# Performance work log

Measured on AMD Instinct MI355X. Metric: run time of the kernel, lower is better.

The kernel has to match this reference:

```python
import jax, jax.numpy as jnp
import numpy as np

N_USERS = 50000
DEG = 32
N_EDGES = N_USERS * DEG  # 1,600,000
N_SERVERS = 512


def segment_softmax(x, seg, num_segments):
    # PyG-style scatter softmax over segments defined by seg.
    m = jax.ops.segment_max(x, seg, num_segments=num_segments)
    e = jnp.exp(x - m[seg])
    s = jax.ops.segment_sum(e, seg, num_segments=num_segments) + 1e-16
    return e / s[seg]


def setup_inputs() -> dict:
    key = jax.random.key(0)
    k1, k2, k3, k4, k5, k6, k7 = jax.random.split(key, 7)
    # learned parameters (torch.rand init), shape [E, 1]
    task_allocation = jax.random.uniform(k1, (N_EDGES, 1), dtype=jnp.float32)
    power_allocation = jax.random.uniform(k2, (N_EDGES, 1), dtype=jnp.float32)
    comp_allocation = jax.random.uniform(k3, (N_EDGES, 1), dtype=jnp.float32)
    compute_resource = jax.random.uniform(k4, (N_SERVERS,), dtype=jnp.float32) + 0.5
    path_losses = jax.random.uniform(k5, (N_EDGES,), dtype=jnp.float32) + 0.1
    task_size = jax.random.uniform(k6, (N_USERS,), dtype=jnp.float32) + 0.1
    # user index sorted (each user has DEG edges); server index random
    user_index = jnp.repeat(jnp.arange(N_USERS, dtype=jnp.int64), DEG)
    server_index = jax.random.randint(k7, (N_EDGES,), 0, N_SERVERS, dtype=jnp.int64)
    edge_index = jnp.stack([user_index, server_index], axis=0)
    return {
        "compute_resource": compute_resource,
        "path_losses": path_losses,
        "task_size": task_size,
        "edge_index": edge_index,
        "task_allocation": task_allocation,
        "power_allocation": power_allocation,
        "comp_allocation": comp_allocation,
    }


def reference(compute_resource, path_losses, task_size, edge_index,
              task_allocation, power_allocation, comp_allocation):
    epsilon = 1e-9
    extre = 1e-20
    n_users = task_size.shape[0]
    n_servers = compute_resource.shape[0]
    user_index = edge_index[0]
    server_index = edge_index[1]

    task_sche = segment_softmax(task_allocation[:, 0], user_index, n_users)
    power_sche = segment_softmax(power_allocation[:, 0], user_index, n_users)
    comp_sche = segment_softmax(comp_allocation[:, 0], user_index, n_users)

    tasks = task_size[user_index] * task_sche            # [E]
    comp = compute_resource[server_index] * comp_sche     # [E]
    pw = power_sche * path_losses                         # [E]

    # per-server total received power, broadcast back to edges
    pws = jax.ops.segment_sum(pw, server_index, num_segments=n_servers)[server_index]
    interference = pws - pw
    rate = jnp.log2(1.0 + pw / (interference + epsilon))

    time_loss = tasks / (rate + extre) + tasks / (comp + extre)  # [E]
    per_user = jax.ops.segment_sum(time_loss, user_index, num_segments=n_users)
    return per_user.mean()
```

## Files before the change

kernel.cpp:

```cpp
#include <hip/hip_runtime.h>
#include <math.h>

#define NSRV 512
#define NB1  256

__device__ __forceinline__ float quad_sum(float v) {
    int x = __float_as_int(v);
    int y = __builtin_amdgcn_update_dpp(0, x, 0xB1, 0xF, 0xF, true);
    v += __int_as_float(y);
    x = __float_as_int(v);
    y = __builtin_amdgcn_update_dpp(0, x, 0x4E, 0xF, 0xF, true);
    v += __int_as_float(y);
    return v;
}

__device__ __forceinline__ float fast_rcp(float x) {
    return __builtin_amdgcn_rcpf(x);
}

__global__ __launch_bounds__(256) void mmse_pws(
    const float* __restrict__ power_alloc,
    const float* __restrict__ path_losses,
    const int*   __restrict__ server_index,
    float*       __restrict__ pws,
    int n_items) {
    __shared__ float bins[NSRV];
    const int tid = threadIdx.x;
    for (int i = tid; i < NSRV; i += 256) bins[i] = 0.0f;
    __syncthreads();

    const float4* pa4 = (const float4*)power_alloc;
    const float4* pl4 = (const float4*)path_losses;
    const int4*   si4 = (const int4*)server_index;

    const int stride = NB1 * 256;
    for (int t = blockIdx.x * 256 + tid; t < n_items; t += stride) {
        float4 a = pa4[2 * t], b = pa4[2 * t + 1];
        float e0 = __expf(a.x), e1 = __expf(a.y), e2 = __expf(a.z), e3 = __expf(a.w);
        float e4 = __expf(b.x), e5 = __expf(b.y), e6 = __expf(b.z), e7 = __expf(b.w);
        float s   = ((e0 + e1) + (e2 + e3)) + ((e4 + e5) + (e6 + e7));
        float inv = fast_rcp(quad_sum(s) + 1e-16f);

        float4 l0 = pl4[2 * t], l1 = pl4[2 * t + 1];
        int4   s0 = si4[2 * t], s1 = si4[2 * t + 1];

        atomicAdd(&bins[s0.x], e0 * inv * l0.x);
        atomicAdd(&bins[s0.y], e1 * inv * l0.y);
        atomicAdd(&bins[s0.z], e2 * inv * l0.z);
        atomicAdd(&bins[s0.w], e3 * inv * l0.w);
        atomicAdd(&bins[s1.x], e4 * inv * l1.x);
        atomicAdd(&bins[s1.y], e5 * inv * l1.y);
        atomicAdd(&bins[s1.z], e6 * inv * l1.z);
        atomicAdd(&bins[s1.w], e7 * inv * l1.w);
    }
    __syncthreads();

    for (int i = tid; i < NSRV; i += 256) atomicAdd(&pws[i], bins[i]);
}

__global__ __launch_bounds__(256) void mmse_loss(
    const float* __restrict__ task_alloc,
    const float* __restrict__ power_alloc,
    const float* __restrict__ comp_alloc,
    const float* __restrict__ path_losses,
    const int*   __restrict__ server_index,
    const float* __restrict__ task_size,
    const float* __restrict__ compute_resource,
    const float* __restrict__ pws,
    float*       __restrict__ out,
    int n_items, float inv_users) {
    __shared__ float s_pws[NSRV], s_cr[NSRV];
    __shared__ float s_blocksum;
    const int tid = threadIdx.x;

    for (int i = tid; i < NSRV; i += 256) {
        s_pws[i] = pws[i];
        s_cr[i]  = compute_resource[i];
    }
    if (tid == 0) s_blocksum = 0.0f;
    __syncthreads();

    const int t = blockIdx.x * 256 + tid;
    float tl = 0.0f;
    if (t < n_items) {
        const float4* ta4 = (const float4*)task_alloc;
        const float4* pa4 = (const float4*)power_alloc;
        const float4* ca4 = (const float4*)comp_alloc;
        const float4* pl4 = (const float4*)path_losses;
        const int4*   si4 = (const int4*)server_index;

        float4 tA = ta4[2 * t], tB = ta4[2 * t + 1];
        float4 pA = pa4[2 * t], pB = pa4[2 * t + 1];
        float4 cA = ca4[2 * t], cB = ca4[2 * t + 1];
        float4 lA = pl4[2 * t], lB = pl4[2 * t + 1];
        int4   sA = si4[2 * t], sB = si4[2 * t + 1];

        float et[8] = {__expf(tA.x), __expf(tA.y), __expf(tA.z), __expf(tA.w),
                       __expf(tB.x), __expf(tB.y), __expf(tB.z), __expf(tB.w)};
        float ep[8] = {__expf(pA.x), __expf(pA.y), __expf(pA.z), __expf(pA.w),
                       __expf(pB.x), __expf(pB.y), __expf(pB.z), __expf(pB.w)};
        float ec[8] = {__expf(cA.x), __expf(cA.y), __expf(cA.z), __expf(cA.w),
                       __expf(cB.x), __expf(cB.y), __expf(cB.z), __expf(cB.w)};
        float pl[8] = {lA.x, lA.y, lA.z, lA.w, lB.x, lB.y, lB.z, lB.w};
        int   sv[8] = {sA.x, sA.y, sA.z, sA.w, sB.x, sB.y, sB.z, sB.w};

        float st = 0.f, sp = 0.f, sc = 0.f;
#pragma unroll
        for (int k = 0; k < 8; ++k) { st += et[k]; sp += ep[k]; sc += ec[k]; }
        float ist = fast_rcp(quad_sum(st) + 1e-16f);
        float isp = fast_rcp(quad_sum(sp) + 1e-16f);
        float isc = fast_rcp(quad_sum(sc) + 1e-16f);

        const float tsz = task_size[t >> 2];

#pragma unroll
        for (int k = 0; k < 8; ++k) {
            int   srv    = sv[k];
            float tasks  = tsz * (et[k] * ist);
            float comp   = s_cr[srv] * (ec[k] * isc);
            float pwv    = (ep[k] * isp) * pl[k];
            float interf = s_pws[srv] - pwv;
            float rate   = __log2f(1.0f + pwv * fast_rcp(interf + 1e-9f));
            tl += tasks * fast_rcp(rate + 1e-20f) + tasks * fast_rcp(comp + 1e-20f);
        }
    }

    tl = quad_sum(tl);
    if ((tid & 3) == 0 && tl != 0.0f) atomicAdd(&s_blocksum, tl);
    __syncthreads();
    if (tid == 0) atomicAdd(out, s_blocksum * inv_users);
}

extern "C" void kernel_launch(void* const* d_in, const int* in_sizes, int n_in,
                              void* d_out, int out_size, void* d_ws, size_t ws_size,
                              hipStream_t stream) {
    const float* compute_resource = (const float*)d_in[0];
    const float* path_losses      = (const float*)d_in[1];
    const float* task_size        = (const float*)d_in[2];
    const int*   edge_index       = (const int*)d_in[3];
    const float* task_alloc       = (const float*)d_in[4];
    const float* power_alloc      = (const float*)d_in[5];
    const float* comp_alloc       = (const float*)d_in[6];

    const int n_edges = in_sizes[1];
    const int n_users = in_sizes[2];
    const int* server_index = edge_index + n_edges;

    const int n_items = n_edges / 8;
    float* pws = (float*)d_ws;

    mmse_pws<<<NB1, 256, 0, stream>>>(
        power_alloc, path_losses, server_index, pws, n_items);

    const int NB2 = (n_items + 255) / 256;
    mmse_loss<<<NB2, 256, 0, stream>>>(
        task_alloc, power_alloc, comp_alloc, path_losses, server_index,
        task_size, compute_resource, pws, (float*)d_out,
        n_items, 1.0f / (float)n_users);
}
```

Baseline: 111.1 us.

## Fuse power-sum and loss kernels into one persistent kernel with grid barrier

Merges the per-server power histogram kernel and the loss kernel into a single persistent kernel of 256 blocks. Each thread keeps its per-edge power values and server indices in registers across a software grid barrier, built from atomic counters in the workspace, so power_alloc, path_losses and server_index are read only once. Task and compute allocations are prefetched before the barrier to overlap their loads with the synchronization. The cost is lower occupancy (launch bounds of 1 block, 256 blocks total), heavy register pressure, and reliance on all blocks being co-resident and on the barrier words starting out zeroed.

Result: slower. 139.5 us (+25.5%).

```diff
diff --git a/kernel.cpp b/kernel.cpp
--- a/kernel.cpp
+++ b/kernel.cpp
@@ -1,8 +1,10 @@
 #include <hip/hip_runtime.h>
 #include <math.h>
 
-#define NSRV 512
-#define NB1  256
+#define NSRV  512
+#define NBLK  256
+#define NTHR  256
+#define MAGIC 0x13579BDF
 
 __device__ __forceinline__ float quad_sum(float v) {
     int x = __float_as_int(v);
@@ -18,47 +20,7 @@
     return __builtin_amdgcn_rcpf(x);
 }
 
-__global__ __launch_bounds__(256) void mmse_pws(
-    const float* __restrict__ power_alloc,
-    const float* __restrict__ path_losses,
-    const int*   __restrict__ server_index,
-    float*       __restrict__ pws,
-    int n_items) {
-    __shared__ float bins[NSRV];
-    const int tid = threadIdx.x;
-    for (int i = tid; i < NSRV; i += 256) bins[i] = 0.0f;
-    __syncthreads();
-
-    const float4* pa4 = (const float4*)power_alloc;
-    const float4* pl4 = (const float4*)path_losses;
-    const int4*   si4 = (const int4*)server_index;
-
-    const int stride = NB1 * 256;
-    for (int t = blockIdx.x * 256 + tid; t < n_items; t += stride) {
-        float4 a = pa4[2 * t], b = pa4[2 * t + 1];
-        float e0 = __expf(a.x), e1 = __expf(a.y), e2 = __expf(a.z), e3 = __expf(a.w);
-        float e4 = __expf(b.x), e5 = __expf(b.y), e6 = __expf(b.z), e7 = __expf(b.w);
-        float s   = ((e0 + e1) + (e2 + e3)) + ((e4 + e5) + (e6 + e7));
-        float inv = fast_rcp(quad_sum(s) + 1e-16f);
-
-        float4 l0 = pl4[2 * t], l1 = pl4[2 * t + 1];
-        int4   s0 = si4[2 * t], s1 = si4[2 * t + 1];
-
-        atomicAdd(&bins[s0.x], e0 * inv * l0.x);
-        atomicAdd(&bins[s0.y], e1 * inv * l0.y);
-        atomicAdd(&bins[s0.z], e2 * inv * l0.z);
-        atomicAdd(&bins[s0.w], e3 * inv * l0.w);
-        atomicAdd(&bins[s1.x], e4 * inv * l1.x);
-        atomicAdd(&bins[s1.y], e5 * inv * l1.y);
-        atomicAdd(&bins[s1.z], e6 * inv * l1.z);
-        atomicAdd(&bins[s1.w], e7 * inv * l1.w);
-    }
-    __syncthreads();
-
-    for (int i = tid; i < NSRV; i += 256) atomicAdd(&pws[i], bins[i]);
-}
-
-__global__ __launch_bounds__(256) void mmse_loss(
+__global__ __launch_bounds__(NTHR, 1) void mmse_fused(
     const float* __restrict__ task_alloc,
     const float* __restrict__ power_alloc,
     const float* __restrict__ comp_alloc,
@@ -66,62 +28,124 @@
     const int*   __restrict__ server_index,
     const float* __restrict__ task_size,
     const float* __restrict__ compute_resource,
-    const float* __restrict__ pws,
+    float*       __restrict__ pws,
+    int*         __restrict__ sync_ws,
     float*       __restrict__ out,
     int n_items, float inv_users) {
-    __shared__ float s_pws[NSRV], s_cr[NSRV];
+    __shared__ float bins[NSRV];
+    __shared__ float s_pws[NSRV];
+    __shared__ float s_cr[NSRV];
     __shared__ float s_blocksum;
     const int tid = threadIdx.x;
 
-    for (int i = tid; i < NSRV; i += 256) {
-        s_pws[i] = pws[i];
-        s_cr[i]  = compute_resource[i];
+    for (int i = tid; i < NSRV; i += NTHR) {
+        bins[i] = 0.0f;
+        s_cr[i] = compute_resource[i];
     }
     if (tid == 0) s_blocksum = 0.0f;
     __syncthreads();
 
-    const int t = blockIdx.x * 256 + tid;
-    float tl = 0.0f;
-    if (t < n_items) {
-        const float4* ta4 = (const float4*)task_alloc;
-        const float4* pa4 = (const float4*)power_alloc;
-        const float4* ca4 = (const float4*)comp_alloc;
-        const float4* pl4 = (const float4*)path_losses;
-        const int4*   si4 = (const int4*)server_index;
+    const int g      = blockIdx.x * NTHR + tid;
+    const int stride = NBLK * NTHR;
 
-        float4 tA = ta4[2 * t], tB = ta4[2 * t + 1];
-        float4 pA = pa4[2 * t], pB = pa4[2 * t + 1];
-        float4 cA = ca4[2 * t], cB = ca4[2 * t + 1];
-        float4 lA = pl4[2 * t], lB = pl4[2 * t + 1];
-        int4   sA = si4[2 * t], sB = si4[2 * t + 1];
+    const float4* pa4 = (const float4*)power_alloc;
+    const float4* pl4 = (const float4*)path_losses;
+    const int4*   si4 = (const int4*)server_index;
+    const float4* ta4 = (const float4*)task_alloc;
+    const float4* ca4 = (const float4*)comp_alloc;
 
-        float et[8] = {__expf(tA.x), __expf(tA.y), __expf(tA.z), __expf(tA.w),
-                       __expf(tB.x), __expf(tB.y), __expf(tB.z), __expf(tB.w)};
-        float ep[8] = {__expf(pA.x), __expf(pA.y), __expf(pA.z), __expf(pA.w),
-                       __expf(pB.x), __expf(pB.y), __expf(pB.z), __expf(pB.w)};
-        float ec[8] = {__expf(cA.x), __expf(cA.y), __expf(cA.z), __expf(cA.w),
-                       __expf(cB.x), __expf(cB.y), __expf(cB.z), __expf(cB.w)};
-        float pl[8] = {lA.x, lA.y, lA.z, lA.w, lB.x, lB.y, lB.z, lB.w};
-        int   sv[8] = {sA.x, sA.y, sA.z, sA.w, sB.x, sB.y, sB.z, sB.w};
-
-        float st = 0.f, sp = 0.f, sc = 0.f;
-#pragma unroll
-        for (int k = 0; k < 8; ++k) { st += et[k]; sp += ep[k]; sc += ec[k]; }
-        float ist = fast_rcp(quad_sum(st) + 1e-16f);
-        float isp = fast_rcp(quad_sum(sp) + 1e-16f);
-        float isc = fast_rcp(quad_sum(sc) + 1e-16f);
-
-        const float tsz = task_size[t >> 2];
+    float  pwv[4][8];
+    int    srv[4][8];
+    float4 tA[4], tB[4], cA[4], cB[4];
+    float  tsz[4];
+    bool   valid[4];
 
 #pragma unroll
-        for (int k = 0; k < 8; ++k) {
-            int   srv    = sv[k];
-            float tasks  = tsz * (et[k] * ist);
-            float comp   = s_cr[srv] * (ec[k] * isc);
-            float pwv    = (ep[k] * isp) * pl[k];
-            float interf = s_pws[srv] - pwv;
-            float rate   = __log2f(1.0f + pwv * fast_rcp(interf + 1e-9f));
-            tl += tasks * fast_rcp(rate + 1e-20f) + tasks * fast_rcp(comp + 1e-20f);
+    for (int k = 0; k < 4; ++k) {
+        const int t = g + k * stride;
+        valid[k] = (k < 3) || (t < n_items);
+        if (valid[k]) {
+            float4 a  = pa4[2 * t], b  = pa4[2 * t + 1];
+            float4 l0 = pl4[2 * t], l1 = pl4[2 * t + 1];
+            int4   s0 = si4[2 * t], s1 = si4[2 * t + 1];
+            float e0 = __expf(a.x), e1 = __expf(a.y), e2 = __expf(a.z), e3 = __expf(a.w);
+            float e4 = __expf(b.x), e5 = __expf(b.y), e6 = __expf(b.z), e7 = __expf(b.w);
+            float s   = ((e0 + e1) + (e2 + e3)) + ((e4 + e5) + (e6 + e7));
+            float inv = fast_rcp(quad_sum(s) + 1e-16f);
+
+            pwv[k][0] = e0 * inv * l0.x; pwv[k][1] = e1 * inv * l0.y;
+            pwv[k][2] = e2 * inv * l0.z; pwv[k][3] = e3 * inv * l0.w;
+            pwv[k][4] = e4 * inv * l1.x; pwv[k][5] = e5 * inv * l1.y;
+            pwv[k][6] = e6 * inv * l1.z; pwv[k][7] = e7 * inv * l1.w;
+            srv[k][0] = s0.x; srv[k][1] = s0.y; srv[k][2] = s0.z; srv[k][3] = s0.w;
+            srv[k][4] = s1.x; srv[k][5] = s1.y; srv[k][6] = s1.z; srv[k][7] = s1.w;
+#pragma unroll
+            for (int e = 0; e < 8; ++e) atomicAdd(&bins[srv[k][e]], pwv[k][e]);
+        }
+    }
+
+#pragma unroll
+    for (int k = 0; k < 4; ++k) {
+        const int t = g + k * stride;
+        if (valid[k]) {
+            tA[k] = ta4[2 * t]; tB[k] = ta4[2 * t + 1];
+            cA[k] = ca4[2 * t]; cB[k] = ca4[2 * t + 1];
+            tsz[k] = task_size[t >> 2];
+        }
+    }
+
+    __syncthreads();
+    for (int i = tid; i < NSRV; i += NTHR) atomicAdd(&pws[i], bins[i]);
+    __threadfence();
+    __syncthreads();
+
+    if (tid == 0) {
+        if (blockIdx.x == 0) {
+            __hip_atomic_store(&sync_ws[0], 0, __ATOMIC_RELAXED,
+                               __HIP_MEMORY_SCOPE_AGENT);
+            __hip_atomic_store(&sync_ws[1], MAGIC, __ATOMIC_RELEASE,
+                               __HIP_MEMORY_SCOPE_AGENT);
+        } else {
+            while (__hip_atomic_load(&sync_ws[1], __ATOMIC_ACQUIRE,
+                                     __HIP_MEMORY_SCOPE_AGENT) != MAGIC)
+                __builtin_amdgcn_s_sleep(8);
+        }
+        atomicAdd(&sync_ws[0], 1);
+        while (__hip_atomic_load(&sync_ws[0], __ATOMIC_ACQUIRE,
+                                 __HIP_MEMORY_SCOPE_AGENT) < NBLK)
+            __builtin_amdgcn_s_sleep(8);
+    }
+    __syncthreads();
+
+    for (int i = tid; i < NSRV; i += NTHR)
+        s_pws[i] = __hip_atomic_load(&pws[i], __ATOMIC_RELAXED,
+                                     __HIP_MEMORY_SCOPE_AGENT);
+    __syncthreads();
+
+    float tl = 0.0f;
+#pragma unroll
+    for (int k = 0; k < 4; ++k) {
+        if (valid[k]) {
+            float et[8] = {__expf(tA[k].x), __expf(tA[k].y), __expf(tA[k].z), __expf(tA[k].w),
+                           __expf(tB[k].x), __expf(tB[k].y), __expf(tB[k].z), __expf(tB[k].w)};
+            float ec[8] = {__expf(cA[k].x), __expf(cA[k].y), __expf(cA[k].z), __expf(cA[k].w),
+                           __expf(cB[k].x), __expf(cB[k].y), __expf(cB[k].z), __expf(cB[k].w)};
+            float st = 0.f, sc = 0.f;
+#pragma unroll
+            for (int e = 0; e < 8; ++e) { st += et[e]; sc += ec[e]; }
+            float ist = fast_rcp(quad_sum(st) + 1e-16f);
+            float isc = fast_rcp(quad_sum(sc) + 1e-16f);
+
+#pragma unroll
+            for (int e = 0; e < 8; ++e) {
+                int   sv     = srv[k][e];
+                float tasks  = tsz[k] * (et[e] * ist);
+                float comp   = s_cr[sv] * (ec[e] * isc);
+                float p      = pwv[k][e];
+                float interf = s_pws[sv] - p;
+                float rate   = __log2f(1.0f + p * fast_rcp(interf + 1e-9f));
+                tl += tasks * fast_rcp(rate + 1e-20f) + tasks * fast_rcp(comp + 1e-20f);
+            }
         }
     }
 
@@ -147,14 +171,11 @@
     const int* server_index = edge_index + n_edges;
 
     const int n_items = n_edges / 8;
-    float* pws = (float*)d_ws;
+    float* pws     = (float*)d_ws;
+    int*   sync_ws = (int*)(pws + NSRV);
 
-    mmse_pws<<<NB1, 256, 0, stream>>>(
-        power_alloc, path_losses, server_index, pws, n_items);
-
-    const int NB2 = (n_items + 255) / 256;
-    mmse_loss<<<NB2, 256, 0, stream>>>(
+    mmse_fused<<<NBLK, NTHR, 0, stream>>>(
         task_alloc, power_alloc, comp_alloc, path_losses, server_index,
-        task_size, compute_resource, pws, (float*)d_out,
+        task_size, compute_resource, pws, sync_ws, (float*)d_out,
         n_items, 1.0f / (float)n_users);
 }
```
